# Kernel tuning notes

Hardware: AMD Instinct MI355X
Metric: run time of the kernel (lower is better)

The kernel has to match this reference:

```python
import jax, jax.numpy as jnp
import numpy as np

NEG_SLOPE = 0.2

def _gat_layer(x, src, dst, W, a_s, a_d, b, concat):
    # x: [N, F_in], W: [F_in, H*C], a_s/a_d: [H, C]
    N = x.shape[0]
    H, C = a_s.shape
    h = (x @ W).reshape(N, H, C)                       # per-head projection
    al_s = jnp.sum(h * a_s, axis=-1)                   # [N, H]
    al_d = jnp.sum(h * a_d, axis=-1)                   # [N, H]
    e = jax.nn.leaky_relu(al_s[src] + al_d[dst], NEG_SLOPE)  # [E, H]
    # segment softmax over incoming edges of each dst node
    m = jax.ops.segment_max(e, dst, num_segments=N)    # [N, H]
    ex = jnp.exp(e - m[dst])
    denom = jax.ops.segment_sum(ex, dst, num_segments=N)
    alpha = ex / denom[dst]                            # [E, H]
    msg = h[src] * alpha[:, :, None]                   # [E, H, C]
    out = jax.ops.segment_sum(msg, dst, num_segments=N)  # [N, H, C]
    if concat:
        return out.reshape(N, H * C) + b
    return out.mean(axis=1) + b


def setup_inputs() -> dict:
    key = jax.random.key(0)
    ks = jax.random.split(key, 12)
    N, F_in, H, C1, LAT, E = 16384, 512, 4, 128, 64, 262144
    x = jax.random.normal(ks[0], (N, F_in), dtype=jnp.float32)
    edge_index = jax.random.randint(ks[1], (2, E), 0, N, dtype=jnp.int64)
    s = 0.05
    return {
        'x': x,
        'edge_index': edge_index,
        'W1': jax.random.normal(ks[2], (F_in, H * C1), dtype=jnp.float32) * s,
        'a_src1': jax.random.normal(ks[3], (H, C1), dtype=jnp.float32) * s,
        'a_dst1': jax.random.normal(ks[4], (H, C1), dtype=jnp.float32) * s,
        'b1': jax.random.normal(ks[5], (H * C1,), dtype=jnp.float32) * s,
        'W2': jax.random.normal(ks[6], (H * C1, H * LAT), dtype=jnp.float32) * s,
        'a_src2': jax.random.normal(ks[7], (H, LAT), dtype=jnp.float32) * s,
        'a_dst2': jax.random.normal(ks[8], (H, LAT), dtype=jnp.float32) * s,
        'b2': jax.random.normal(ks[9], (LAT,), dtype=jnp.float32) * s,
    }


def reference(x, edge_index, W1, a_src1, a_dst1, b1, W2, a_src2, a_dst2, b2):
    N = x.shape[0]
    # PyG GATConv default add_self_loops=True
    loop = jnp.arange(N, dtype=edge_index.dtype)
    src = jnp.concatenate([edge_index[0], loop])
    dst = jnp.concatenate([edge_index[1], loop])
    h = jax.nn.relu(_gat_layer(x, src, dst, W1, a_src1, a_dst1, b1, concat=True))
    out = _gat_layer(h, src, dst, W2, a_src2, a_dst2, b2, concat=False)
    return out
```

## Files before the change

### kernel.cpp

```cpp
#include <hip/hip_runtime.h>
#include <stdint.h>
#include <stddef.h>
#include <limits.h>

typedef __bf16 bf16;
typedef __bf16 bf16x4 __attribute__((ext_vector_type(4)));
typedef __bf16 bf16x8 __attribute__((ext_vector_type(8)));
typedef float  f32x4  __attribute__((ext_vector_type(4)));

#define CAP 128

static __device__ __forceinline__ float lrelu(float x) { return x > 0.f ? x : 0.2f * x; }
static __device__ __forceinline__ float san(float v) { return (fabsf(v) < 1e4f) ? v : 0.0f; }
static __device__ __forceinline__ float wexp(float e) { return __expf(fminf(e, 30.f)); }

static __device__ __forceinline__ void async_load16(const bf16* g, bf16* l) {
  __builtin_amdgcn_global_load_lds((const __attribute__((address_space(1))) void*)g,
                                   (__attribute__((address_space(3))) void*)l, 16, 0, 0);
}

static __device__ __forceinline__ void drain_barrier() {
  asm volatile("s_waitcnt vmcnt(0) lgkmcnt(0)" ::: "memory");
  __builtin_amdgcn_s_barrier();
}


__global__ __launch_bounds__(256) void prep_w(int* __restrict__ cnt,
                                              const float* __restrict__ W1,
                                              const float* __restrict__ W2,
                                              bf16* __restrict__ W1T,
                                              bf16* __restrict__ W2T,
                                              int N) {
  int b = blockIdx.x;
  if (b < N / 256) { cnt[b * 256 + threadIdx.x] = 0; return; }
  b -= N / 256;
  __shared__ bf16 t[32][33];
  const float* in; bf16* out; int R, C, bx, by;
  if (b < 256) { in = W1; out = W1T; R = 512; C = 512; by = b >> 4; bx = b & 15; }
  else         { b -= 256; in = W2; out = W2T; R = 512; C = 256; by = b >> 3; bx = b & 7; }
  const int lane = threadIdx.x & 31, r8 = threadIdx.x >> 5;
#pragma unroll
  for (int k = 0; k < 4; ++k) {
    int r = by * 32 + r8 + k * 8, c = bx * 32 + lane;
    t[lane][r8 + k * 8] = (bf16)san(in[(size_t)r * C + c]);
  }
  __syncthreads();
#pragma unroll
  for (int k = 0; k < 4; ++k) {
    int oc = bx * 32 + r8 + k * 8;
    out[(size_t)oc * R + by * 32 + lane] = t[r8 + k * 8][lane];
  }
}


__global__ __launch_bounds__(256) void gemm_al_l1(const float* __restrict__ X,
                                                  const bf16* __restrict__ BT,
                                                  bf16* __restrict__ C,
                                                  const float* __restrict__ a_s,
                                                  const float* __restrict__ a_d,
                                                  float* __restrict__ al_s,
                                                  float* __restrict__ al_d,
                                                  const int* __restrict__ src,
                                                  const int* __restrict__ dst,
                                                  int E, int* __restrict__ cnt,
                                                  int* __restrict__ slots,
                                                  int M, int N, int K) {
  __shared__ __align__(16) bf16 As[2][64 * 32];
  __shared__ __align__(16) bf16 Bs[2][128 * 32];
  __shared__ float alred[2][64][2];
  const int tid = threadIdx.x;
  const int b   = blockIdx.x;

  if (b >= 1024) {
    for (int e = (b - 1024) * 256 + tid; e < E; e += 512 * 256) {
      int d = dst[e];
      int pos = atomicAdd(&cnt[d], 1);
      if (pos < CAP) slots[(size_t)d * CAP + pos] = src[e];
    }
    return;
  }

  const int lane = tid & 63;
  const int wave = tid >> 6;
  const int m0 = (b & 255) * 64;
  const int head = b >> 8;
  const int n0 = head * 128;
  const int wm = (wave >> 1) * 32;
  const int wn = (wave & 1) * 64;

  f32x4 acc[2][4] = {};

  const int id1 = tid + 256;
  const float* apx = X  + (size_t)(m0 + (tid >> 2)) * K + (tid & 3) * 8;
  const bf16*  b0p = BT + (size_t)(n0 + (tid >> 2)) * K + (tid & 3) * 8;
  const bf16*  b1p = BT + (size_t)(n0 + (id1 >> 2)) * K + (id1 & 3) * 8;

  const int kq = (lane >> 4) * 8;
  const int rA = wm + (lane & 15);
  const int rB = wn + (lane & 15);

  {
    f32x4 u0 = *(const f32x4*)(apx);
    f32x4 u1 = *(const f32x4*)(apx + 4);
    async_load16(b0p, &Bs[0][tid * 8]);
    async_load16(b1p, &Bs[0][id1 * 8]);
    bf16x8 w;
#pragma unroll
    for (int k = 0; k < 4; ++k) { w[k] = (bf16)san(u0[k]); w[4 + k] = (bf16)san(u1[k]); }
    *(bf16x8*)&As[0][tid * 8] = w;
    drain_barrier();
  }

  int cur = 0;
  for (int k0 = 0; k0 < K; k0 += 32) {
    const int kn = (k0 + 32 < K) ? (k0 + 32) : k0;
    f32x4 u0 = *(const f32x4*)(apx + kn);
    f32x4 u1 = *(const f32x4*)(apx + kn + 4);
    async_load16(b0p + kn, &Bs[cur ^ 1][tid * 8]);
    async_load16(b1p + kn, &Bs[cur ^ 1][id1 * 8]);

    bf16x8 af[2], bfv[4];
#pragma unroll
    for (int i = 0; i < 2; ++i) af[i]  = *(const bf16x8*)&As[cur][(rA + i * 16) * 32 + kq];
#pragma unroll
    for (int j = 0; j < 4; ++j) bfv[j] = *(const bf16x8*)&Bs[cur][(rB + j * 16) * 32 + kq];
#pragma unroll
    for (int i = 0; i < 2; ++i)
#pragma unroll
      for (int j = 0; j < 4; ++j)
        acc[i][j] = __builtin_amdgcn_mfma_f32_16x16x32_bf16(af[i], bfv[j], acc[i][j], 0, 0, 0);

    bf16x8 w;
#pragma unroll
    for (int k = 0; k < 4; ++k) { w[k] = (bf16)san(u0[k]); w[4 + k] = (bf16)san(u1[k]); }
    *(bf16x8*)&As[cur ^ 1][tid * 8] = w;

    drain_barrier();
    cur ^= 1;
  }

  const int cc = lane & 15;
  const int rb = (lane >> 4) * 4;
#pragma unroll
  for (int i = 0; i < 2; ++i)
#pragma unroll
    for (int j = 0; j < 4; ++j) {
      int gcol = n0 + wn + j * 16 + cc;
#pragma unroll
      for (int r = 0; r < 4; ++r) {
        int grow = m0 + wm + i * 16 + rb + r;
        C[(size_t)grow * N + gcol] = (bf16)acc[i][j][r];
      }
    }

  {
    float asv[4], adv[4];
#pragma unroll
    for (int j = 0; j < 4; ++j) {
      int col = head * 128 + wn + j * 16 + cc;
      asv[j] = san(a_s[col]);
      adv[j] = san(a_d[col]);
    }
    const int wnh = wn >> 6;
#pragma unroll
    for (int i = 0; i < 2; ++i)
#pragma unroll
      for (int r = 0; r < 4; ++r) {
        float ps = 0.f, pd = 0.f;
#pragma unroll
        for (int j = 0; j < 4; ++j) { ps += acc[i][j][r] * asv[j]; pd += acc[i][j][r] * adv[j]; }
#pragma unroll
        for (int off = 1; off <= 8; off <<= 1) {
          ps += __shfl_xor(ps, off);
          pd += __shfl_xor(pd, off);
        }
        if (cc == 0) {
          int row = wm + i * 16 + rb + r;
          alred[wnh][row][0] = ps;
          alred[wnh][row][1] = pd;
        }
      }
    __syncthreads();
    if (tid < 64) {
      al_s[(size_t)(m0 + tid) * 4 + head] = alred[0][tid][0] + alred[1][tid][0];
      al_d[(size_t)(m0 + tid) * 4 + head] = alred[0][tid][1] + alred[1][tid][1];
    }
  }
}


__global__ __launch_bounds__(256) void gemm_al_l2(const bf16* __restrict__ A,
                                                  const bf16* __restrict__ BT,
                                                  bf16* __restrict__ C,
                                                  const float* __restrict__ a_s,
                                                  const float* __restrict__ a_d,
                                                  float* __restrict__ al_s,
                                                  float* __restrict__ al_d,
                                                  int M, int N, int K) {
  __shared__ __align__(16) bf16 As[2][64 * 32];
  __shared__ __align__(16) bf16 Bs[2][64 * 32];
  __shared__ float alred[2][64][2];
  const int tid  = threadIdx.x;
  const int lane = tid & 63;
  const int wave = tid >> 6;
  const int m0   = blockIdx.x * 64;
  const int head = blockIdx.y;
  const int n0   = head * 64;
  const int wm = (wave >> 1) * 32;
  const int wn = (wave & 1) * 32;

  f32x4 acc[2][2] = {};

  const bf16* ap = A  + (size_t)(m0 + (tid >> 2)) * K + (tid & 3) * 8;
  const bf16* bp = BT + (size_t)(n0 + (tid >> 2)) * K + (tid & 3) * 8;

  const int kq = (lane >> 4) * 8;
  const int rA = wm + (lane & 15);
  const int rB = wn + (lane & 15);

  async_load16(ap, &As[0][tid * 8]);
  async_load16(bp, &Bs[0][tid * 8]);
  drain_barrier();

  int cur = 0;
  for (int k0 = 0; k0 < K; k0 += 32) {
    const int kn = (k0 + 32 < K) ? (k0 + 32) : k0;
    async_load16(ap + kn, &As[cur ^ 1][tid * 8]);
    async_load16(bp + kn, &Bs[cur ^ 1][tid * 8]);

    bf16x8 af[2], bfv[2];
#pragma unroll
    for (int i = 0; i < 2; ++i) af[i]  = *(const bf16x8*)&As[cur][(rA + i * 16) * 32 + kq];
#pragma unroll
    for (int j = 0; j < 2; ++j) bfv[j] = *(const bf16x8*)&Bs[cur][(rB + j * 16) * 32 + kq];
#pragma unroll
    for (int i = 0; i < 2; ++i)
#pragma unroll
      for (int j = 0; j < 2; ++j)
        acc[i][j] = __builtin_amdgcn_mfma_f32_16x16x32_bf16(af[i], bfv[j], acc[i][j], 0, 0, 0);

    drain_barrier();
    cur ^= 1;
  }

  const int cc = lane & 15;
  const int rb = (lane >> 4) * 4;
#pragma unroll
  for (int i = 0; i < 2; ++i)
#pragma unroll
    for (int j = 0; j < 2; ++j) {
      int gcol = n0 + wn + j * 16 + cc;
#pragma unroll
      for (int r = 0; r < 4; ++r) {
        int grow = m0 + wm + i * 16 + rb + r;
        C[(size_t)grow * N + gcol] = (bf16)acc[i][j][r];
      }
    }

  {
    float asv[2], adv[2];
#pragma unroll
    for (int j = 0; j < 2; ++j) {
      int col = n0 + wn + j * 16 + cc;
      asv[j] = san(a_s[col]);
      adv[j] = san(a_d[col]);
    }
    const int wnh = wn >> 5;
#pragma unroll
    for (int i = 0; i < 2; ++i)
#pragma unroll
      for (int r = 0; r < 4; ++r) {
        float ps = 0.f, pd = 0.f;
#pragma unroll
        for (int j = 0; j < 2; ++j) { ps += acc[i][j][r] * asv[j]; pd += acc[i][j][r] * adv[j]; }
#pragma unroll
        for (int off = 1; off <= 8; off <<= 1) {
          ps += __shfl_xor(ps, off);
          pd += __shfl_xor(pd, off);
        }
        if (cc == 0) {
          int row = wm + i * 16 + rb + r;
          alred[wnh][row][0] = ps;
          alred[wnh][row][1] = pd;
        }
      }
    __syncthreads();
    if (tid < 64) {
      al_s[(size_t)(m0 + tid) * 4 + head] = alred[0][tid][0] + alred[1][tid][0];
      al_d[(size_t)(m0 + tid) * 4 + head] = alred[0][tid][1] + alred[1][tid][1];
    }
  }
}


__global__ __launch_bounds__(256) void sort_mkL(const float* __restrict__ al_s,
                                                const float* __restrict__ al_d,
                                                const int* __restrict__ cnt,
                                                int* __restrict__ slots,
                                                float* __restrict__ Linv) {
  const int wv   = threadIdx.x >> 6;
  const int lane = threadIdx.x & 63;
  const int n = blockIdx.x * 4 + wv;
  const int beg = n * CAP;
  const int len = min(cnt[n], CAP);
  const f32x4 alsn = *(const f32x4*)(al_s + (size_t)n * 4);
  const f32x4 aldn = *(const f32x4*)(al_d + (size_t)n * 4);

  f32x4 L = {0.f, 0.f, 0.f, 0.f};
  if (lane == 0) {
#pragma unroll
    for (int h = 0; h < 4; ++h) L[h] = wexp(lrelu(alsn[h] + aldn[h]));
  }

  if (len <= 64) {
    int v = (lane < len) ? slots[beg + lane] : INT_MAX;
    if (len > 1) {
#pragma unroll
      for (int k = 2; k <= 64; k <<= 1) {
#pragma unroll
        for (int j = k >> 1; j > 0; j >>= 1) {
          int p = __shfl_xor(v, j);
          bool take_min = (((lane & k) == 0) == ((lane & j) == 0));
          v = take_min ? min(v, p) : max(v, p);
        }
      }
      if (lane < len) slots[beg + lane] = v;
    }
    if (lane < len) {
      f32x4 a = *(const f32x4*)(al_s + (size_t)v * 4);
#pragma unroll
      for (int h = 0; h < 4; ++h) L[h] += wexp(lrelu(a[h] + aldn[h]));
    }
  } else {
    if (lane == 0) {
      for (int i = beg + 1; i < beg + len; ++i) {
        int v = slots[i];
        int j = i - 1;
        while (j >= beg && slots[j] > v) { slots[j + 1] = slots[j]; --j; }
        slots[j + 1] = v;
      }
    }
    asm volatile("s_waitcnt vmcnt(0)" ::: "memory");
    for (int c0 = beg; c0 < beg + len; c0 += 64) {
      const int cl = min(64, beg + len - c0);
      if (lane < cl) {
        int s = slots[c0 + lane];
        f32x4 a = *(const f32x4*)(al_s + (size_t)s * 4);
#pragma unroll
        for (int h = 0; h < 4; ++h) L[h] += wexp(lrelu(a[h] + aldn[h]));
      }
    }
  }

  for (int off = 32; off; off >>= 1) {
#pragma unroll
    for (int h = 0; h < 4; ++h) L[h] += __shfl_xor(L[h], off);
  }
  if (lane == 0) {
    f32x4 o;
#pragma unroll
    for (int h = 0; h < 4; ++h) o[h] = 1.0f / L[h];
    *(f32x4*)(Linv + (size_t)n * 4) = o;
  }
}


__global__ __launch_bounds__(256) void aggregate1_s(const bf16* __restrict__ h1,
                                                    const float* __restrict__ al_s,
                                                    const float* __restrict__ al_d,
                                                    const int* __restrict__ cnt,
                                                    const int* __restrict__ slots,
                                                    const float* __restrict__ Linv,
                                                    const float* __restrict__ bias,
                                                    bf16* __restrict__ out) {
  const int sl   = blockIdx.x & 7;
  const int g    = blockIdx.x >> 3;
  const int wv   = threadIdx.x >> 6;
  const int lane = threadIdx.x & 63;
  const int n    = g * 4 + wv;
  const int hd   = sl >> 1;
  const int c8   = lane & 7;
  const int sub  = lane >> 3;
  const int cbase = sl * 64 + c8 * 8;
  const int beg = n * CAP;
  const int len = min(cnt[n], CAP);
  const float aldh = al_d[(size_t)n * 4 + hd];

  float acc[8] = {};
  if (sub == 0) {
    float wself = wexp(lrelu(al_s[(size_t)n * 4 + hd] + aldh));
    bf16x8 hv = *(const bf16x8*)(h1 + (size_t)n * 512 + cbase);
#pragma unroll
    for (int k = 0; k < 8; ++k) acc[k] = wself * (float)hv[k];
  }

  for (int c0 = 0; c0 < len; c0 += 64) {
    const int cl = min(64, len - c0);
    int v = (lane < cl) ? slots[beg + c0 + lane] : 0;
    float wl = 0.f;
    if (lane < cl) wl = wexp(lrelu(al_s[(size_t)v * 4 + hd] + aldh));
    for (int j0 = 0; j0 < cl; j0 += 8) {
      int jj = j0 + sub;
      int   sj = __shfl(v, jj);
      float wj = __shfl(wl, jj);
      bf16x8 rv = *(const bf16x8*)(h1 + (size_t)sj * 512 + cbase);
#pragma unroll
      for (int k = 0; k < 8; ++k) acc[k] += wj * (float)rv[k];
    }
  }

#pragma unroll
  for (int off = 8; off <= 32; off <<= 1)
#pragma unroll
    for (int k = 0; k < 8; ++k) acc[k] += __shfl_xor(acc[k], off);

  if (sub == 0) {
    const float inv = Linv[(size_t)n * 4 + hd];
    bf16x8 ov;
#pragma unroll
    for (int k = 0; k < 8; ++k)
      ov[k] = (bf16)fmaxf(acc[k] * inv + san(bias[cbase + k]), 0.f);
    *(bf16x8*)(out + (size_t)n * 512 + cbase) = ov;
  }
}


__global__ __launch_bounds__(256) void aggregate2_f(const bf16* __restrict__ h2,
                                                    const float* __restrict__ al_s,
                                                    const float* __restrict__ al_d,
                                                    const int* __restrict__ cnt,
                                                    const int* __restrict__ slots,
                                                    const float* __restrict__ bias,
                                                    float* __restrict__ out) {
  __shared__ int   sIdx[4][64];
  __shared__ f32x4 sW[4][64];
  const int wv   = threadIdx.x >> 6;
  const int lane = threadIdx.x & 63;
  const int n = blockIdx.x * 4 + wv;
  const int hd = lane >> 4;
  const int cb = lane * 4;
  const int beg = n * CAP;
  const int len = min(cnt[n], CAP);
  const f32x4 alsn = *(const f32x4*)(al_s + (size_t)n * 4);
  const f32x4 aldn = *(const f32x4*)(al_d + (size_t)n * 4);

  const float wself = wexp(lrelu(alsn[hd] + aldn[hd]));
  bf16x4 hv0 = *(const bf16x4*)(h2 + (size_t)n * 256 + cb);
  float acc0 = wself * (float)hv0[0], acc1 = wself * (float)hv0[1];
  float acc2 = wself * (float)hv0[2], acc3 = wself * (float)hv0[3];
  f32x4 Lv = {0.f, 0.f, 0.f, 0.f};
  if (lane == 0) {
#pragma unroll
    for (int h = 0; h < 4; ++h) Lv[h] = wexp(lrelu(alsn[h] + aldn[h]));
  }
  for (int c0 = beg; c0 < beg + len; c0 += 64) {
    const int cl = min(64, beg + len - c0);
    if (lane < cl) {
      int s = slots[c0 + lane];
      sIdx[wv][lane] = s;
      f32x4 a = *(const f32x4*)(al_s + (size_t)s * 4);
      f32x4 w;
#pragma unroll
      for (int h = 0; h < 4; ++h) w[h] = wexp(lrelu(a[h] + aldn[h]));
      sW[wv][lane] = w;
#pragma unroll
      for (int h = 0; h < 4; ++h) Lv[h] += w[h];
    }
    for (int j0 = 0; j0 < cl; j0 += 8) {
      bf16x4 rv[8];
      float  wt[8];
#pragma unroll
      for (int t = 0; t < 8; ++t) {
        int jj = j0 + t;
        int s  = sIdx[wv][jj < cl ? jj : cl - 1];
        rv[t]  = *(const bf16x4*)(h2 + (size_t)s * 256 + cb);
        wt[t]  = (jj < cl) ? sW[wv][jj][hd] : 0.f;
      }
#pragma unroll
      for (int t = 0; t < 8; ++t) {
        acc0 += wt[t] * (float)rv[t][0];
        acc1 += wt[t] * (float)rv[t][1];
        acc2 += wt[t] * (float)rv[t][2];
        acc3 += wt[t] * (float)rv[t][3];
      }
    }
  }
  for (int off = 32; off; off >>= 1) {
#pragma unroll
    for (int h = 0; h < 4; ++h) Lv[h] += __shfl_xor(Lv[h], off);
  }
  const float inv = 1.0f / Lv[hd];
  acc0 *= inv; acc1 *= inv; acc2 *= inv; acc3 *= inv;
  acc0 += __shfl_xor(acc0, 16); acc1 += __shfl_xor(acc1, 16);
  acc2 += __shfl_xor(acc2, 16); acc3 += __shfl_xor(acc3, 16);
  acc0 += __shfl_xor(acc0, 32); acc1 += __shfl_xor(acc1, 32);
  acc2 += __shfl_xor(acc2, 32); acc3 += __shfl_xor(acc3, 32);
  if (lane < 16) {
    int ob = lane * 4;
    f32x4 ov;
    ov[0] = 0.25f * acc0 + san(bias[ob]);
    ov[1] = 0.25f * acc1 + san(bias[ob + 1]);
    ov[2] = 0.25f * acc2 + san(bias[ob + 2]);
    ov[3] = 0.25f * acc3 + san(bias[ob + 3]);
    *(f32x4*)(out + (size_t)n * 64 + ob) = ov;
  }
}


extern "C" void kernel_launch(void* const* d_in, const int* in_sizes, int n_in,
                              void* d_out, int out_size, void* d_ws, size_t ws_size,
                              hipStream_t stream) {
  const float* x   = (const float*)d_in[0];
  const int*   ei  = (const int*)d_in[1];
  const float* W1  = (const float*)d_in[2];
  const float* as1 = (const float*)d_in[3];
  const float* ad1 = (const float*)d_in[4];
  const float* b1  = (const float*)d_in[5];
  const float* W2  = (const float*)d_in[6];
  const float* as2 = (const float*)d_in[7];
  const float* ad2 = (const float*)d_in[8];
  const float* b2  = (const float*)d_in[9];
  float* outp = (float*)d_out;

  const int N = in_sizes[0] / 512;
  const int E = in_sizes[1] / 2;
  const int* src = ei;
  const int* dst = ei + E;

  char* p = (char*)d_ws;
  auto alloc = [&](size_t bytes) {
    char* r = p;
    p += (bytes + 255) & ~(size_t)255;
    return r;
  };
  bf16* h1    = (bf16*)alloc((size_t)N * 512 * 2);
  bf16* hbuf  = (bf16*)alloc((size_t)N * 512 * 2);
  bf16* W1T   = (bf16*)alloc((size_t)512 * 512 * 2);
  bf16* W2T   = (bf16*)alloc((size_t)256 * 512 * 2);
  float* al_s1 = (float*)alloc((size_t)N * 4 * 4);
  float* al_d1 = (float*)alloc((size_t)N * 4 * 4);
  float* al_s2 = (float*)alloc((size_t)N * 4 * 4);
  float* al_d2 = (float*)alloc((size_t)N * 4 * 4);
  float* Linv1 = (float*)alloc((size_t)N * 4 * 4);
  int* cnt     = (int*)alloc((size_t)N * 4);
  int* slots   = (int*)alloc((size_t)N * CAP * 4);
  bf16* h2 = h1;

  prep_w<<<N / 256 + 256 + 128, 256, 0, stream>>>(cnt, W1, W2, W1T, W2T, N);

  gemm_al_l1<<<1024 + 512, 256, 0, stream>>>(x, W1T, h1, as1, ad1, al_s1, al_d1,
                                             src, dst, E, cnt, slots, N, 512, 512);
  sort_mkL<<<N / 4, 256, 0, stream>>>(al_s1, al_d1, cnt, slots, Linv1);
  aggregate1_s<<<8 * (N / 4), 256, 0, stream>>>(h1, al_s1, al_d1, cnt, slots, Linv1,
                                                b1, hbuf);

  gemm_al_l2<<<dim3(N / 64, 4), 256, 0, stream>>>(hbuf, W2T, h2, as2, ad2, al_s2, al_d2,
                                                  N, 256, 512);
  aggregate2_f<<<N / 4, 256, 0, stream>>>(h2, al_s2, al_d2, cnt, slots, b2, outp);
}
```

Measured before the change: 215.0 us.

## Map aggregation blocks to XCDs by head and split layer-2 aggregation per head

```diff
diff --git a/kernel.cpp b/kernel.cpp
--- a/kernel.cpp
+++ b/kernel.cpp
@@ -297,7 +297,8 @@
                                                 const float* __restrict__ al_d,
                                                 const int* __restrict__ cnt,
                                                 int* __restrict__ slots,
-                                                float* __restrict__ Linv) {
+                                                float* __restrict__ Linv,
+                                                int do_sort) {
   const int wv   = threadIdx.x >> 6;
   const int lane = threadIdx.x & 63;
   const int n = blockIdx.x * 4 + wv;
@@ -314,7 +315,7 @@
 
   if (len <= 64) {
     int v = (lane < len) ? slots[beg + lane] : INT_MAX;
-    if (len > 1) {
+    if (do_sort && len > 1) {
 #pragma unroll
       for (int k = 2; k <= 64; k <<= 1) {
 #pragma unroll
@@ -332,7 +333,7 @@
       for (int h = 0; h < 4; ++h) L[h] += wexp(lrelu(a[h] + aldn[h]));
     }
   } else {
-    if (lane == 0) {
+    if (do_sort && lane == 0) {
       for (int i = beg + 1; i < beg + len; ++i) {
         int v = slots[i];
         int j = i - 1;
@@ -373,15 +374,16 @@
                                                     const float* __restrict__ Linv,
                                                     const float* __restrict__ bias,
                                                     bf16* __restrict__ out) {
-  const int sl   = blockIdx.x & 7;
-  const int g    = blockIdx.x >> 3;
+  const int xcd  = blockIdx.x & 7;
+  const int hd   = xcd >> 1;
+  const int par  = xcd & 1;
+  const int g    = (blockIdx.x >> 3) * 2 + par;
   const int wv   = threadIdx.x >> 6;
   const int lane = threadIdx.x & 63;
   const int n    = g * 4 + wv;
-  const int hd   = sl >> 1;
-  const int c8   = lane & 7;
-  const int sub  = lane >> 3;
-  const int cbase = sl * 64 + c8 * 8;
+  const int c16  = lane & 15;
+  const int sub  = lane >> 4;
+  const int cbase = hd * 128 + c16 * 8;
   const int beg = n * CAP;
   const int len = min(cnt[n], CAP);
   const float aldh = al_d[(size_t)n * 4 + hd];
@@ -396,14 +398,73 @@
 
   for (int c0 = 0; c0 < len; c0 += 64) {
     const int cl = min(64, len - c0);
-    int v = (lane < cl) ? slots[beg + c0 + lane] : 0;
-    float wl = 0.f;
-    if (lane < cl) wl = wexp(lrelu(al_s[(size_t)v * 4 + hd] + aldh));
+    int   v  = (lane < cl) ? slots[beg + c0 + lane] : 0;
+    float wl = (lane < cl) ? wexp(lrelu(al_s[(size_t)v * 4 + hd] + aldh)) : 0.f;
+    for (int j0 = 0; j0 < cl; j0 += 4) {
+      int jj = j0 + sub;
+      int   sj = __shfl(v, jj);
+      float wj = __shfl(wl, jj);
+      bf16x8 rv = *(const bf16x8*)(h1 + (size_t)sj * 512 + cbase);
+#pragma unroll
+      for (int k = 0; k < 8; ++k) acc[k] += wj * (float)rv[k];
+    }
+  }
+
+#pragma unroll
+  for (int off = 16; off <= 32; off <<= 1)
+#pragma unroll
+    for (int k = 0; k < 8; ++k) acc[k] += __shfl_xor(acc[k], off);
+
+  if (sub == 0) {
+    const float inv = Linv[(size_t)n * 4 + hd];
+    bf16x8 ov;
+#pragma unroll
+    for (int k = 0; k < 8; ++k)
+      ov[k] = (bf16)fmaxf(acc[k] * inv + san(bias[cbase + k]), 0.f);
+    *(bf16x8*)(out + (size_t)n * 512 + cbase) = ov;
+  }
+}
+
+
+__global__ __launch_bounds__(256) void aggregate2_s(const bf16* __restrict__ h2,
+                                                    const float* __restrict__ al_s,
+                                                    const float* __restrict__ al_d,
+                                                    const int* __restrict__ cnt,
+                                                    const int* __restrict__ slots,
+                                                    const float* __restrict__ Linv,
+                                                    float* __restrict__ partials,
+                                                    int N) {
+  const int xcd  = blockIdx.x & 7;
+  const int hd   = xcd >> 1;
+  const int par  = xcd & 1;
+  const int g    = (blockIdx.x >> 3) * 2 + par;
+  const int wv   = threadIdx.x >> 6;
+  const int lane = threadIdx.x & 63;
+  const int n    = g * 4 + wv;
+  const int c8   = lane & 7;
+  const int sub  = lane >> 3;
+  const int cbase = hd * 64 + c8 * 8;
+  const int beg = n * CAP;
+  const int len = min(cnt[n], CAP);
+  const float aldh = al_d[(size_t)n * 4 + hd];
+
+  float acc[8] = {};
+  if (sub == 0) {
+    float wself = wexp(lrelu(al_s[(size_t)n * 4 + hd] + aldh));
+    bf16x8 hv = *(const bf16x8*)(h2 + (size_t)n * 256 + cbase);
+#pragma unroll
+    for (int k = 0; k < 8; ++k) acc[k] = wself * (float)hv[k];
+  }
+
+  for (int c0 = 0; c0 < len; c0 += 64) {
+    const int cl = min(64, len - c0);
+    int   v  = (lane < cl) ? slots[beg + c0 + lane] : 0;
+    float wl = (lane < cl) ? wexp(lrelu(al_s[(size_t)v * 4 + hd] + aldh)) : 0.f;
     for (int j0 = 0; j0 < cl; j0 += 8) {
       int jj = j0 + sub;
       int   sj = __shfl(v, jj);
       float wj = __shfl(wl, jj);
-      bf16x8 rv = *(const bf16x8*)(h1 + (size_t)sj * 512 + cbase);
+      bf16x8 rv = *(const bf16x8*)(h2 + (size_t)sj * 256 + cbase);
 #pragma unroll
       for (int k = 0; k < 8; ++k) acc[k] += wj * (float)rv[k];
     }
@@ -416,94 +477,32 @@
 
   if (sub == 0) {
     const float inv = Linv[(size_t)n * 4 + hd];
-    bf16x8 ov;
-#pragma unroll
-    for (int k = 0; k < 8; ++k)
-      ov[k] = (bf16)fmaxf(acc[k] * inv + san(bias[cbase + k]), 0.f);
-    *(bf16x8*)(out + (size_t)n * 512 + cbase) = ov;
-  }
-}
-
-
-__global__ __launch_bounds__(256) void aggregate2_f(const bf16* __restrict__ h2,
-                                                    const float* __restrict__ al_s,
-                                                    const float* __restrict__ al_d,
-                                                    const int* __restrict__ cnt,
-                                                    const int* __restrict__ slots,
-                                                    const float* __restrict__ bias,
-                                                    float* __restrict__ out) {
-  __shared__ int   sIdx[4][64];
-  __shared__ f32x4 sW[4][64];
-  const int wv   = threadIdx.x >> 6;
-  const int lane = threadIdx.x & 63;
-  const int n = blockIdx.x * 4 + wv;
-  const int hd = lane >> 4;
-  const int cb = lane * 4;
-  const int beg = n * CAP;
-  const int len = min(cnt[n], CAP);
-  const f32x4 alsn = *(const f32x4*)(al_s + (size_t)n * 4);
-  const f32x4 aldn = *(const f32x4*)(al_d + (size_t)n * 4);
-
-  const float wself = wexp(lrelu(alsn[hd] + aldn[hd]));
-  bf16x4 hv0 = *(const bf16x4*)(h2 + (size_t)n * 256 + cb);
-  float acc0 = wself * (float)hv0[0], acc1 = wself * (float)hv0[1];
-  float acc2 = wself * (float)hv0[2], acc3 = wself * (float)hv0[3];
-  f32x4 Lv = {0.f, 0.f, 0.f, 0.f};
-  if (lane == 0) {
-#pragma unroll
-    for (int h = 0; h < 4; ++h) Lv[h] = wexp(lrelu(alsn[h] + aldn[h]));
-  }
-  for (int c0 = beg; c0 < beg + len; c0 += 64) {
-    const int cl = min(64, beg + len - c0);
-    if (lane < cl) {
-      int s = slots[c0 + lane];
-      sIdx[wv][lane] = s;
-      f32x4 a = *(const f32x4*)(al_s + (size_t)s * 4);
-      f32x4 w;
-#pragma unroll
-      for (int h = 0; h < 4; ++h) w[h] = wexp(lrelu(a[h] + aldn[h]));
-      sW[wv][lane] = w;
-#pragma unroll
-      for (int h = 0; h < 4; ++h) Lv[h] += w[h];
-    }
-    for (int j0 = 0; j0 < cl; j0 += 8) {
-      bf16x4 rv[8];
-      float  wt[8];
-#pragma unroll
-      for (int t = 0; t < 8; ++t) {
-        int jj = j0 + t;
-        int s  = sIdx[wv][jj < cl ? jj : cl - 1];
-        rv[t]  = *(const bf16x4*)(h2 + (size_t)s * 256 + cb);
-        wt[t]  = (jj < cl) ? sW[wv][jj][hd] : 0.f;
-      }
-#pragma unroll
-      for (int t = 0; t < 8; ++t) {
-        acc0 += wt[t] * (float)rv[t][0];
-        acc1 += wt[t] * (float)rv[t][1];
-        acc2 += wt[t] * (float)rv[t][2];
-        acc3 += wt[t] * (float)rv[t][3];
-      }
-    }
-  }
-  for (int off = 32; off; off >>= 1) {
-#pragma unroll
-    for (int h = 0; h < 4; ++h) Lv[h] += __shfl_xor(Lv[h], off);
-  }
-  const float inv = 1.0f / Lv[hd];
-  acc0 *= inv; acc1 *= inv; acc2 *= inv; acc3 *= inv;
-  acc0 += __shfl_xor(acc0, 16); acc1 += __shfl_xor(acc1, 16);
-  acc2 += __shfl_xor(acc2, 16); acc3 += __shfl_xor(acc3, 16);
-  acc0 += __shfl_xor(acc0, 32); acc1 += __shfl_xor(acc1, 32);
-  acc2 += __shfl_xor(acc2, 32); acc3 += __shfl_xor(acc3, 32);
-  if (lane < 16) {
-    int ob = lane * 4;
-    f32x4 ov;
-    ov[0] = 0.25f * acc0 + san(bias[ob]);
-    ov[1] = 0.25f * acc1 + san(bias[ob + 1]);
-    ov[2] = 0.25f * acc2 + san(bias[ob + 2]);
-    ov[3] = 0.25f * acc3 + san(bias[ob + 3]);
-    *(f32x4*)(out + (size_t)n * 64 + ob) = ov;
-  }
+    float* p = partials + ((size_t)hd * N + n) * 64 + c8 * 8;
+    f32x4 o0, o1;
+#pragma unroll
+    for (int k = 0; k < 4; ++k) { o0[k] = acc[k] * inv; o1[k] = acc[4 + k] * inv; }
+    *(f32x4*)(p)     = o0;
+    *(f32x4*)(p + 4) = o1;
+  }
+}
+
+
+__global__ __launch_bounds__(256) void combine2(const float* __restrict__ partials,
+                                                const float* __restrict__ bias,
+                                                float* __restrict__ out, int N) {
+  int i = blockIdx.x * 256 + threadIdx.x;
+  int idx = i * 4;
+  int n = idx >> 6, c = idx & 63;
+  const size_t plane = (size_t)N * 64;
+  f32x4 p0 = *(const f32x4*)(partials + 0 * plane + (size_t)n * 64 + c);
+  f32x4 p1 = *(const f32x4*)(partials + 1 * plane + (size_t)n * 64 + c);
+  f32x4 p2 = *(const f32x4*)(partials + 2 * plane + (size_t)n * 64 + c);
+  f32x4 p3 = *(const f32x4*)(partials + 3 * plane + (size_t)n * 64 + c);
+  f32x4 o;
+#pragma unroll
+  for (int k = 0; k < 4; ++k)
+    o[k] = 0.25f * (p0[k] + p1[k] + p2[k] + p3[k]) + san(bias[c + k]);
+  *(f32x4*)(out + idx) = o;
 }
 
 
@@ -542,19 +541,24 @@
   float* al_s2 = (float*)alloc((size_t)N * 4 * 4);
   float* al_d2 = (float*)alloc((size_t)N * 4 * 4);
   float* Linv1 = (float*)alloc((size_t)N * 4 * 4);
+  float* Linv2 = (float*)alloc((size_t)N * 4 * 4);
   int* cnt     = (int*)alloc((size_t)N * 4);
   int* slots   = (int*)alloc((size_t)N * CAP * 4);
+  float* part2 = (float*)alloc((size_t)4 * N * 64 * 4);
   bf16* h2 = h1;
 
   prep_w<<<N / 256 + 256 + 128, 256, 0, stream>>>(cnt, W1, W2, W1T, W2T, N);
 
   gemm_al_l1<<<1024 + 512, 256, 0, stream>>>(x, W1T, h1, as1, ad1, al_s1, al_d1,
                                              src, dst, E, cnt, slots, N, 512, 512);
-  sort_mkL<<<N / 4, 256, 0, stream>>>(al_s1, al_d1, cnt, slots, Linv1);
-  aggregate1_s<<<8 * (N / 4), 256, 0, stream>>>(h1, al_s1, al_d1, cnt, slots, Linv1,
+  sort_mkL<<<N / 4, 256, 0, stream>>>(al_s1, al_d1, cnt, slots, Linv1, 1);
+  aggregate1_s<<<8 * (N / 8), 256, 0, stream>>>(h1, al_s1, al_d1, cnt, slots, Linv1,
                                                 b1, hbuf);
 
   gemm_al_l2<<<dim3(N / 64, 4), 256, 0, stream>>>(hbuf, W2T, h2, as2, ad2, al_s2, al_d2,
                                                   N, 256, 512);
-  aggregate2_f<<<N / 4, 256, 0, stream>>>(h2, al_s2, al_d2, cnt, slots, b2, outp);
-}
+  sort_mkL<<<N / 4, 256, 0, stream>>>(al_s2, al_d2, cnt, slots, Linv2, 0);
+  aggregate2_s<<<8 * (N / 8), 256, 0, stream>>>(h2, al_s2, al_d2, cnt, slots, Linv2,
+                                                part2, N);
+  combine2<<<(N * 64 / 4) / 256, 256, 0, stream>>>(part2, b2, outp, N);
+}
```

Result: no change. 217.8 us (+1.3%).
